# Kernel optimization log

Hardware: AMD Instinct MI355X
Metric: run time of the kernel (lower is better)

The kernel has to match this reference:

```python
import jax, jax.numpy as jnp
import numpy as np

N, C_IN, T, V = 128, 64, 64, 25
K = 3           # num_subsets
C_OUT = 192
MID = 64        # int((1/K) * C_OUT)
EPS = 1e-5


def conv1x1(x, W, b):
    # x: (n,c,t,v), W: (o,c), b: (o,)  -> (n,o,t,v)
    return jnp.einsum('nctv,oc->notv', x, W) + b[None, :, None, None]


def bn_eval(x, p):
    # p: (4,C) rows = gamma, beta, running_mean, running_var
    g, b, m, v = p[0], p[1], p[2], p[3]
    scale = (g * jax.lax.rsqrt(v + EPS))[None, :, None, None]
    return x * scale + (b - m * g * jax.lax.rsqrt(v + EPS))[None, :, None, None]


def _bn_params(key, c):
    kg, kb, km, kv = jax.random.split(key, 4)
    return jnp.stack([
        1.0 + 0.1 * jax.random.normal(kg, (c,), jnp.float32),
        0.1 * jax.random.normal(kb, (c,), jnp.float32),
        0.1 * jax.random.normal(km, (c,), jnp.float32),
        0.5 + jax.random.uniform(kv, (c,), jnp.float32),
    ])


def setup_inputs() -> dict:
    key = jax.random.key(0)
    ks = jax.random.split(key, 20)
    rn = lambda k, shape, s=1.0: s * jax.random.normal(k, shape, jnp.float32)
    return {
        'x': rn(ks[0], (N, C_IN, T, V)),
        'A': rn(ks[1], (K, V, V), 0.1),
        'alpha': rn(ks[2], (K,), 0.1),
        'beta': rn(ks[3], (K,), 0.1),
        'W_pre': rn(ks[4], (MID * K, C_IN), 0.05), 'b_pre': rn(ks[5], (MID * K,), 0.05),
        'bn_pre': _bn_params(ks[6], MID * K),
        'W1': rn(ks[7], (MID * K, C_IN), 0.05), 'b1': rn(ks[8], (MID * K,), 0.05),
        'W2': rn(ks[9], (MID * K, C_IN), 0.05), 'b2': rn(ks[10], (MID * K,), 0.05),
        'W_post': rn(ks[11], (C_OUT, MID * K), 0.05), 'b_post': rn(ks[12], (C_OUT,), 0.05),
        'bn_post': _bn_params(ks[13], C_OUT),
        'W_down': rn(ks[14], (C_OUT, C_IN), 0.05), 'b_down': rn(ks[15], (C_OUT,), 0.05),
        'bn_down': _bn_params(ks[16], C_OUT),
    }


def reference(x, A, alpha, beta, W_pre, b_pre, bn_pre, W1, b1, W2, b2,
              W_post, b_post, bn_post, W_down, b_down, bn_down):
    n = x.shape[0]
    # residual branch (in_channels != out_channels -> conv + BN)
    res = bn_eval(conv1x1(x, W_down, b_down), bn_down)
    # pre: conv1x1 -> BN -> ReLU, reshaped to (n,k,mid,t,v)
    pre_x = jax.nn.relu(bn_eval(conv1x1(x, W_pre, b_pre), bn_pre)).reshape(n, K, MID, T, V)
    # ctr/ada both active and neither 'NA' -> temporal mean
    tmp = x.mean(axis=2, keepdims=True)                      # (n,c,1,v)
    x1 = conv1x1(tmp, W1, b1).reshape(n, K, MID, 1, V)       # (n,k,mid,1,v)
    x2 = conv1x1(tmp, W2, b2).reshape(n, K, MID, 1, V)
    # ctr branch: tanh(pairwise diff) * alpha[0], added to static A
    diff = jnp.tanh(x1[..., :, None] - x2[..., None, :]) * alpha[0]   # (n,k,mid,1,v,v)
    Adyn = diff + A[None, :, None, None]                              # broadcast (1,k,1,1,v,v)
    # ada branch: softmax(x1^T x2) over axis -2, scaled by beta[0]
    ada = jnp.einsum('nkctv,nkctw->nktvw', x1, x2)[:, :, None]        # (n,k,1,1,v,v)
    ada = jax.nn.softmax(ada, axis=-2) * beta[0]
    Adyn = Adyn + ada                                                 # (n,k,mid,1,v,v)
    # A.shape[3] == 1 path: squeeze t-dim, channel-wise adjacency
    Adyn = Adyn[:, :, :, 0]                                           # (n,k,mid,v,v)
    y = jnp.einsum('nkctv,nkcvw->nkctw', pre_x, Adyn).reshape(n, K * MID, T, V)
    y = conv1x1(y, W_post, b_post)
    return jax.nn.relu(bn_eval(y, bn_post) + res)
```

## Files before the change

kernel.cpp:

```cpp
#include <hip/hip_runtime.h>
#include <hip/hip_bf16.h>

typedef __hip_bfloat16 bf16;
typedef __attribute__((ext_vector_type(8))) short s16x8;
typedef __attribute__((ext_vector_type(4))) float f32x4;

constexpr int cN = 128, cC = 64, cT = 64, cV = 25, cK = 3, cMID = 64, cKM = 192, cTV = 1600;
constexpr float cEPS = 1e-5f;

__device__ float g_tmp[cN * cC * cV];
__device__ ushort g_adF[(size_t)cN * cKM * 1024];
__device__ ushort g_WpreF[2 * 12 * 512];
__device__ ushort g_WcatF[8 * 12 * 512];
__device__ float g_bpre [cKM];
__device__ float g_cterm[cKM];

__device__ __forceinline__ ushort f2bu(float v){ return __builtin_bit_cast(ushort, __float2bfloat16(v)); }

__device__ __forceinline__ int zidx(int oct, int col){
  return (oct*128 + (col ^ ((oct & 3) << 1))) * 8;
}

__global__ __launch_bounds__(256) void gm_tmp(const float* __restrict__ x,
    const float* __restrict__ Wpre, const float* __restrict__ bpre,
    const float* __restrict__ bnpre,
    const float* __restrict__ Wpost, const float* __restrict__ bpost,
    const float* __restrict__ bnpost,
    const float* __restrict__ Wdown, const float* __restrict__ bdown,
    const float* __restrict__ bndown){
  __shared__ float xs[4 * cTV];
  int n = blockIdx.x >> 4, cg = blockIdx.x & 15;
  int tid = threadIdx.x;
  const float* xp = x + ((size_t)n*cC + cg*4)*cTV;
  for (int i = tid; i < 4*cTV; i += 256) xs[i] = xp[i];
  __syncthreads();
  if (tid < 100){
    int c = tid / 25, v = tid - c*25;
    float s = 0.f;
    #pragma unroll
    for (int t = 0; t < cT; ++t) s += xs[c*cTV + t*cV + v];
    g_tmp[(n*cC + cg*4 + c)*cV + v] = s * (1.f/cT);
  }
  if (blockIdx.x >= 8) return;
  __syncthreads();
  float* sPre  = xs;
  float* sPost = xs + 32;
  float* sDown = xs + 64;
  int ob = blockIdx.x * 24;
  if (tid < 24){
    int o = ob + tid;
    float sp = bnpre[o] * rsqrtf(bnpre[3*cKM+o] + cEPS);
    sPre[tid] = sp;
    g_bpre[o] = bpre[o]*sp + bnpre[cKM+o] - bnpre[2*cKM+o]*sp;
    float sP = bnpost[o] * rsqrtf(bnpost[3*cKM+o] + cEPS);
    float sD = bndown[o] * rsqrtf(bndown[3*cKM+o] + cEPS);
    sPost[tid] = sP; sDown[tid] = sD;
    g_cterm[o] = bpost[o]*sP + bnpost[cKM+o] - bnpost[2*cKM+o]*sP
               + bdown[o]*sD + bndown[cKM+o] - bndown[2*cKM+o]*sD;
  }
  __syncthreads();
  for (int i = tid; i < 24*cC; i += 256){
    int ol = i >> 6, k = i & 63;
    int o = ob + ol;
    int step = k >> 5, g = (k >> 3) & 3, j = k & 7;
    int dst = ((step*12 + (o>>4)) << 9) + (((g<<4) | (o&15)) << 3) + j;
    g_WpreF[dst] = f2bu(Wpre[o*cC + k] * sPre[ol]);
  }
  for (int i = tid; i < 24*256; i += 256){
    int ol = i >> 8, k = i & 255;
    int o = ob + ol;
    float w = (k < cKM) ? Wpost[o*cKM + k] * sPost[ol]
                        : Wdown[o*cC + (k - cKM)] * sDown[ol];
    int step = k >> 5, g = (k >> 3) & 3, j = k & 7;
    int dst = ((step*12 + (o>>4)) << 9) + (((g<<4) | (o&15)) << 3) + j;
    g_WcatF[dst] = f2bu(w);
  }
}

__global__ __launch_bounds__(512) void gm_prep(
    const float* __restrict__ W1, const float* __restrict__ b1,
    const float* __restrict__ W2, const float* __restrict__ b2,
    const float* __restrict__ A,  const float* __restrict__ alpha,
    const float* __restrict__ beta){
  __shared__ float tl [cC*cV + 32];
  __shared__ float w1l[cMID*65];
  __shared__ float w2l[cMID*65];
  __shared__ float x1l[cMID*cV];
  __shared__ float x2l[cMID*cV];
  __shared__ float Al [cV*cV];
  __shared__ float adal[cV*cV];
  int bid = blockIdx.x; int n = bid / 3, kg = bid % 3;
  int tid = threadIdx.x;
  for (int i = tid; i < cC*cV; i += 512) tl[i] = g_tmp[n*cC*cV + i];
  if (tid < 32) tl[cC*cV + tid] = 0.f;
  for (int i = tid; i < cV*cV; i += 512) Al[i] = A[kg*625 + i];
  for (int i = tid; i < cMID*cC; i += 512){
    int ch = i >> 6, c = i & 63;
    w1l[ch*65 + c] = W1[(kg*cMID + ch)*cC + c];
    w2l[ch*65 + c] = W2[(kg*cMID + ch)*cC + c];
  }
  __syncthreads();
  {
    int ch = tid >> 3, iv = tid & 7;
    int o = kg*cMID + ch;
    float bb1 = b1[o], bb2 = b2[o];
    float s1[4] = {bb1, bb1, bb1, bb1};
    float s2[4] = {bb2, bb2, bb2, bb2};
    #pragma unroll 8
    for (int c = 0; c < cC; ++c){
      float w1c = w1l[ch*65 + c], w2c = w2l[ch*65 + c];
      #pragma unroll
      for (int k = 0; k < 4; ++k){
        float t = tl[c*cV + iv + 8*k];
        s1[k] += w1c * t;
        s2[k] += w2c * t;
      }
    }
    #pragma unroll
    for (int k = 0; k < 4; ++k){
      int v = iv + 8*k;
      if (v < cV){ x1l[ch*cV + v] = s1[k]; x2l[ch*cV + v] = s2[k]; }
    }
  }
  __syncthreads();
  for (int idx = tid; idx < cV*cV; idx += 512){
    int v = idx / cV, w = idx % cV;
    float s = 0.f;
    #pragma unroll 8
    for (int c = 0; c < cMID; ++c) s += x1l[c*cV + v] * x2l[c*cV + w];
    adal[idx] = s;
  }
  __syncthreads();
  float b0 = beta[0];
  if (tid < cV){
    int w = tid;
    float m = -1e30f;
    for (int v = 0; v < cV; ++v) m = fmaxf(m, adal[v*cV + w]);
    float s = 0.f;
    for (int v = 0; v < cV; ++v) s += __expf(adal[v*cV + w] - m);
    float inv = b0 / s;
    for (int v = 0; v < cV; ++v) adal[v*cV + w] = __expf(adal[v*cV + w] - m) * inv;
  }
  __syncthreads();
  for (int i = tid; i < cV*cV; i += 512) Al[i] += adal[i];
  __syncthreads();
  float a0 = alpha[0];
  int rem = tid * 2;
  int nf = rem >> 9, r2 = rem & 511;
  int li = r2 >> 3, j0 = r2 & 7;
  int v0 = 8*(li >> 4) + j0, w = 16*nf + (li & 15);
  bool wok = (w < cV);
  bool v0ok = wok && (v0 < cV), v1ok = wok && (v0 + 1 < cV);
  float AW0 = v0ok ? Al[v0*cV + w] : 0.f;
  float AW1 = v1ok ? Al[(v0+1)*cV + w] : 0.f;
  uint* dst = (uint*)(g_adF + ((size_t)n*cKM + kg*cMID)*1024 + rem);
  #pragma unroll 4
  for (int ch = 0; ch < cMID; ++ch){
    float f0 = 0.f, f1 = 0.f;
    if (wok){
      float xw = x2l[ch*cV + w];
      if (v0ok){
        float e2 = __expf(2.f*(x1l[ch*cV + v0] - xw));
        f0 = __fdividef(e2 - 1.f, e2 + 1.f)*a0 + AW0;
      }
      if (v1ok){
        float e2 = __expf(2.f*(x1l[ch*cV + v0 + 1] - xw));
        f1 = __fdividef(e2 - 1.f, e2 + 1.f)*a0 + AW1;
      }
    }
    dst[(size_t)ch * 512] = (uint)f2bu(f0) | ((uint)f2bu(f1) << 16);
  }
}

__global__ __launch_bounds__(512, 4) void gm_fused(const float* __restrict__ x,
                                                   float* __restrict__ outf){
  __shared__ ushort Zl[32 * 128 * 8];
  __shared__ ushort Pt[64 * 128];
  int c8 = (int)blockIdx.x & 7, i8 = (int)blockIdx.x >> 3;
  int n = c8 + 8*(i8 >> 4), ttile = i8 & 15;
  int t0 = ttile * 4;
  int tid = threadIdx.x;
  int wv = tid >> 6, lane = tid & 63, g = lane >> 4, l15 = lane & 15;
  int mfh = wv >> 1;
  int nfh = wv & 1;

  #pragma unroll
  for (int s0 = 0; s0 < 1024; s0 += 512){
    int s = s0 + tid;
    int oct = 24 + (s >> 7), col = s & 127;
    int t = col >> 5, v = col & 31;
    ushort u[8];
    if (v < cV){
      const float* xp = x + ((size_t)n*cC + (oct-24)*8)*cTV + (t0 + t)*cV + v;
      #pragma unroll
      for (int j = 0; j < 8; ++j) u[j] = f2bu(xp[(size_t)j*cTV]);
    } else {
      #pragma unroll
      for (int j = 0; j < 8; ++j) u[j] = 0;
    }
    *(uint4*)&Zl[zidx(oct, col)] = *(const uint4*)u;
  }

  #pragma unroll 1
  for (int kg = 0; kg < 3; ++kg){
    __syncthreads();
    s16x8 bva0[8], bva1[8];
    #pragma unroll
    for (int cc = 0; cc < 8; ++cc){
      const ushort* bp = g_adF + ((size_t)n*cKM + kg*64 + wv*8 + cc)*1024;
      bva0[cc] = *(const s16x8*)(bp + lane*8);
      bva1[cc] = *(const s16x8*)(bp + 512 + lane*8);
    }
    f32x4 a1[4];
    #pragma unroll
    for (int nn = 0; nn < 4; ++nn) a1[nn] = (f32x4){0.f,0.f,0.f,0.f};
    #pragma unroll
    for (int ks = 0; ks < 2; ++ks){
      s16x8 av = *(const s16x8*)(g_WpreF + ((ks*12 + kg*4 + mfh) << 9) + lane*8);
      #pragma unroll
      for (int nn = 0; nn < 4; ++nn){
        int col = 16*(nfh*4 + nn) + l15;
        s16x8 bv = *(const s16x8*)&Zl[zidx(24 + ks*4 + g, col)];
        a1[nn] = __builtin_amdgcn_mfma_f32_16x16x32_bf16(av, bv, a1[nn], 0, 0, 0);
      }
    }
    #pragma unroll
    for (int nn = 0; nn < 4; ++nn){
      int col = 16*(nfh*4 + nn) + l15;
      int t = col >> 5, v = col & 31;
      #pragma unroll
      for (int q = 0; q < 4; ++q){
        int o = 16*mfh + 4*g + q;
        float val = (v < cV) ? fmaxf(a1[nn][q] + g_bpre[kg*64 + o], 0.f) : 0.f;
        int slot = ((v>>3) ^ (o>>2)) & 3;
        Pt[o*128 + slot*32 + t*8 + (v & 7)] = f2bu(val);
      }
    }
    __syncthreads();
    int octY = kg*8 + wv;
    #pragma unroll
    for (int cc = 0; cc < 8; cc += 2){
      int chlE = wv*8 + cc, chlO = chlE + 1;
      s16x8 avE, avO;
      if (l15 < 4){
        int slotE = (g ^ (chlE>>2)) & 3;
        avE = *(const s16x8*)&Pt[chlE*128 + slotE*32 + l15*8];
        avO = *(const s16x8*)&Pt[chlO*128 + slotE*32 + l15*8];
      } else { avE = (s16x8){0,0,0,0,0,0,0,0}; avO = avE; }
      f32x4 d0e = __builtin_amdgcn_mfma_f32_16x16x32_bf16(avE, bva0[cc],   (f32x4){0.f,0.f,0.f,0.f}, 0, 0, 0);
      f32x4 d1e = __builtin_amdgcn_mfma_f32_16x16x32_bf16(avE, bva1[cc],   (f32x4){0.f,0.f,0.f,0.f}, 0, 0, 0);
      f32x4 d0o = __builtin_amdgcn_mfma_f32_16x16x32_bf16(avO, bva0[cc+1], (f32x4){0.f,0.f,0.f,0.f}, 0, 0, 0);
      f32x4 d1o = __builtin_amdgcn_mfma_f32_16x16x32_bf16(avO, bva1[cc+1], (f32x4){0.f,0.f,0.f,0.f}, 0, 0, 0);
      if (g == 0){
        #pragma unroll
        for (int q = 0; q < 4; ++q){
          uint p0 = (uint)f2bu(d0e[q]) | ((uint)f2bu(d0o[q]) << 16);
          uint p1 = (uint)f2bu(d1e[q]) | ((uint)f2bu(d1o[q]) << 16);
          *(uint*)&Zl[zidx(octY, q*32 + l15)      + cc] = p0;
          *(uint*)&Zl[zidx(octY, q*32 + 16 + l15) + cc] = p1;
        }
      }
    }
  }
  __syncthreads();
  f32x4 a3[3][4];
  #pragma unroll
  for (int mm = 0; mm < 3; ++mm)
    #pragma unroll
    for (int nn = 0; nn < 4; ++nn) a3[mm][nn] = (f32x4){0.f,0.f,0.f,0.f};
  s16x8 avc[3], avn[3];
  #pragma unroll
  for (int mm = 0; mm < 3; ++mm)
    avc[mm] = *(const s16x8*)(g_WcatF + ((0*12 + mfh*3 + mm) << 9) + lane*8);
  #pragma unroll 1
  for (int ks = 0; ks < 8; ++ks){
    if (ks < 7){
      #pragma unroll
      for (int mm = 0; mm < 3; ++mm)
        avn[mm] = *(const s16x8*)(g_WcatF + (((ks+1)*12 + mfh*3 + mm) << 9) + lane*8);
    }
    s16x8 bv[4];
    #pragma unroll
    for (int nn = 0; nn < 4; ++nn){
      int col = 16*(nfh*4 + nn) + l15;
      bv[nn] = *(const s16x8*)&Zl[zidx(ks*4 + g, col)];
    }
    #pragma unroll
    for (int mm = 0; mm < 3; ++mm)
      #pragma unroll
      for (int nn = 0; nn < 4; ++nn)
        a3[mm][nn] = __builtin_amdgcn_mfma_f32_16x16x32_bf16(avc[mm], bv[nn], a3[mm][nn], 0, 0, 0);
    #pragma unroll
    for (int mm = 0; mm < 3; ++mm) avc[mm] = avn[mm];
  }
  #pragma unroll
  for (int mm = 0; mm < 3; ++mm){
    #pragma unroll
    for (int q = 0; q < 4; ++q){
      int o = 48*mfh + 16*mm + 4*g + q;
      float ct = g_cterm[o];
      #pragma unroll
      for (int nn = 0; nn < 4; ++nn){
        int col = 16*(nfh*4 + nn) + l15;
        int t = col >> 5, v = col & 31;
        if (v < cV)
          outf[((size_t)n*cKM + o)*cTV + (t0 + t)*cV + v] = fmaxf(a3[mm][nn][q] + ct, 0.f);
      }
    }
  }
}

extern "C" void kernel_launch(void* const* d_in, const int* in_sizes, int n_in,
                              void* d_out, int out_size, void* d_ws, size_t ws_size,
                              hipStream_t stream){
  (void)in_sizes; (void)n_in; (void)out_size; (void)d_ws; (void)ws_size;
  const float* x      = (const float*)d_in[0];
  const float* A      = (const float*)d_in[1];
  const float* alpha  = (const float*)d_in[2];
  const float* beta   = (const float*)d_in[3];
  const float* W_pre  = (const float*)d_in[4];
  const float* b_pre  = (const float*)d_in[5];
  const float* bn_pre = (const float*)d_in[6];
  const float* W1     = (const float*)d_in[7];
  const float* b1     = (const float*)d_in[8];
  const float* W2     = (const float*)d_in[9];
  const float* b2     = (const float*)d_in[10];
  const float* W_post = (const float*)d_in[11];
  const float* b_post = (const float*)d_in[12];
  const float* bn_post= (const float*)d_in[13];
  const float* W_down = (const float*)d_in[14];
  const float* b_down = (const float*)d_in[15];
  const float* bn_down= (const float*)d_in[16];
  float* out = (float*)d_out;

  gm_tmp  <<<cN * 16,  256, 0, stream>>>(x, W_pre, b_pre, bn_pre,
                                         W_post, b_post, bn_post,
                                         W_down, b_down, bn_down);
  gm_prep <<<cN * 3,   512, 0, stream>>>(W1, b1, W2, b2, A, alpha, beta);
  gm_fused<<<cN * 16,  512, 0, stream>>>(x, out);
}
```

Measured before the change: 161.1 us.

## Interleave post-conv accumulation per subset to halve LDS and raise occupancy

The final post-conv GEMM now accumulates incrementally after each subset's graph aggregation, so only one subset's Y octets plus the x octets have to stay in LDS. This halves the Zl buffer and lets launch bounds request 6 blocks per CU instead of 4. The second half of the adjacency B fragments is now loaded inside the aggregation loop rather than prefetched, which lowers register pressure. In exchange, the a3 accumulators stay live for the whole kernel, each subset needs an extra barrier, and the weight-prefetch pipelining of the old post loop is gone, so register spills or longer latency stalls are possible.

```diff
diff --git a/kernel.cpp b/kernel.cpp
--- a/kernel.cpp
+++ b/kernel.cpp
@@ -172,9 +172,9 @@
   }
 }
 
-__global__ __launch_bounds__(512, 4) void gm_fused(const float* __restrict__ x,
+__global__ __launch_bounds__(512, 6) void gm_fused(const float* __restrict__ x,
                                                    float* __restrict__ outf){
-  __shared__ ushort Zl[32 * 128 * 8];
+  __shared__ ushort Zl[16 * 128 * 8];
   __shared__ ushort Pt[64 * 128];
   int c8 = (int)blockIdx.x & 7, i8 = (int)blockIdx.x >> 3;
   int n = c8 + 8*(i8 >> 4), ttile = i8 & 15;
@@ -187,11 +187,11 @@
   #pragma unroll
   for (int s0 = 0; s0 < 1024; s0 += 512){
     int s = s0 + tid;
-    int oct = 24 + (s >> 7), col = s & 127;
+    int oct = 8 + (s >> 7), col = s & 127;
     int t = col >> 5, v = col & 31;
     ushort u[8];
     if (v < cV){
-      const float* xp = x + ((size_t)n*cC + (oct-24)*8)*cTV + (t0 + t)*cV + v;
+      const float* xp = x + ((size_t)n*cC + (oct-8)*8)*cTV + (t0 + t)*cV + v;
       #pragma unroll
       for (int j = 0; j < 8; ++j) u[j] = f2bu(xp[(size_t)j*cTV]);
     } else {
@@ -200,17 +200,21 @@
     }
     *(uint4*)&Zl[zidx(oct, col)] = *(const uint4*)u;
   }
+
+  f32x4 a3[3][4];
+  #pragma unroll
+  for (int mm = 0; mm < 3; ++mm)
+    #pragma unroll
+    for (int nn = 0; nn < 4; ++nn) a3[mm][nn] = (f32x4){0.f,0.f,0.f,0.f};
 
   #pragma unroll 1
   for (int kg = 0; kg < 3; ++kg){
     __syncthreads();
-    s16x8 bva0[8], bva1[8];
-    #pragma unroll
-    for (int cc = 0; cc < 8; ++cc){
-      const ushort* bp = g_adF + ((size_t)n*cKM + kg*64 + wv*8 + cc)*1024;
-      bva0[cc] = *(const s16x8*)(bp + lane*8);
-      bva1[cc] = *(const s16x8*)(bp + 512 + lane*8);
-    }
+    const ushort* bpBase = g_adF + ((size_t)n*cKM + kg*64 + wv*8)*1024;
+    s16x8 bva0[8];
+    #pragma unroll
+    for (int cc = 0; cc < 8; ++cc)
+      bva0[cc] = *(const s16x8*)(bpBase + cc*1024 + lane*8);
     f32x4 a1[4];
     #pragma unroll
     for (int nn = 0; nn < 4; ++nn) a1[nn] = (f32x4){0.f,0.f,0.f,0.f};
@@ -220,7 +224,7 @@
       #pragma unroll
       for (int nn = 0; nn < 4; ++nn){
         int col = 16*(nfh*4 + nn) + l15;
-        s16x8 bv = *(const s16x8*)&Zl[zidx(24 + ks*4 + g, col)];
+        s16x8 bv = *(const s16x8*)&Zl[zidx(8 + ks*4 + g, col)];
         a1[nn] = __builtin_amdgcn_mfma_f32_16x16x32_bf16(av, bv, a1[nn], 0, 0, 0);
       }
     }
@@ -237,7 +241,6 @@
       }
     }
     __syncthreads();
-    int octY = kg*8 + wv;
     #pragma unroll
     for (int cc = 0; cc < 8; cc += 2){
       int chlE = wv*8 + cc, chlO = chlE + 1;
@@ -247,51 +250,59 @@
         avE = *(const s16x8*)&Pt[chlE*128 + slotE*32 + l15*8];
         avO = *(const s16x8*)&Pt[chlO*128 + slotE*32 + l15*8];
       } else { avE = (s16x8){0,0,0,0,0,0,0,0}; avO = avE; }
+      s16x8 b1e = *(const s16x8*)(bpBase + cc*1024     + 512 + lane*8);
+      s16x8 b1o = *(const s16x8*)(bpBase + (cc+1)*1024 + 512 + lane*8);
       f32x4 d0e = __builtin_amdgcn_mfma_f32_16x16x32_bf16(avE, bva0[cc],   (f32x4){0.f,0.f,0.f,0.f}, 0, 0, 0);
-      f32x4 d1e = __builtin_amdgcn_mfma_f32_16x16x32_bf16(avE, bva1[cc],   (f32x4){0.f,0.f,0.f,0.f}, 0, 0, 0);
+      f32x4 d1e = __builtin_amdgcn_mfma_f32_16x16x32_bf16(avE, b1e,        (f32x4){0.f,0.f,0.f,0.f}, 0, 0, 0);
       f32x4 d0o = __builtin_amdgcn_mfma_f32_16x16x32_bf16(avO, bva0[cc+1], (f32x4){0.f,0.f,0.f,0.f}, 0, 0, 0);
-      f32x4 d1o = __builtin_amdgcn_mfma_f32_16x16x32_bf16(avO, bva1[cc+1], (f32x4){0.f,0.f,0.f,0.f}, 0, 0, 0);
+      f32x4 d1o = __builtin_amdgcn_mfma_f32_16x16x32_bf16(avO, b1o,        (f32x4){0.f,0.f,0.f,0.f}, 0, 0, 0);
       if (g == 0){
         #pragma unroll
         for (int q = 0; q < 4; ++q){
           uint p0 = (uint)f2bu(d0e[q]) | ((uint)f2bu(d0o[q]) << 16);
           uint p1 = (uint)f2bu(d1e[q]) | ((uint)f2bu(d1o[q]) << 16);
-          *(uint*)&Zl[zidx(octY, q*32 + l15)      + cc] = p0;
-          *(uint*)&Zl[zidx(octY, q*32 + 16 + l15) + cc] = p1;
+          *(uint*)&Zl[zidx(wv, q*32 + l15)      + cc] = p0;
+          *(uint*)&Zl[zidx(wv, q*32 + 16 + l15) + cc] = p1;
         }
       }
     }
-  }
-  __syncthreads();
-  f32x4 a3[3][4];
+    __syncthreads();
+    #pragma unroll
+    for (int ks2 = 0; ks2 < 2; ++ks2){
+      int ks3 = kg*2 + ks2;
+      s16x8 avc[3], bv[4];
+      #pragma unroll
+      for (int mm = 0; mm < 3; ++mm)
+        avc[mm] = *(const s16x8*)(g_WcatF + ((ks3*12 + mfh*3 + mm) << 9) + lane*8);
+      #pragma unroll
+      for (int nn = 0; nn < 4; ++nn){
+        int col = 16*(nfh*4 + nn) + l15;
+        bv[nn] = *(const s16x8*)&Zl[zidx(ks2*4 + g, col)];
+      }
+      #pragma unroll
+      for (int mm = 0; mm < 3; ++mm)
+        #pragma unroll
+        for (int nn = 0; nn < 4; ++nn)
+          a3[mm][nn] = __builtin_amdgcn_mfma_f32_16x16x32_bf16(avc[mm], bv[nn], a3[mm][nn], 0, 0, 0);
+    }
+  }
   #pragma unroll
-  for (int mm = 0; mm < 3; ++mm)
-    #pragma unroll
-    for (int nn = 0; nn < 4; ++nn) a3[mm][nn] = (f32x4){0.f,0.f,0.f,0.f};
-  s16x8 avc[3], avn[3];
-  #pragma unroll
-  for (int mm = 0; mm < 3; ++mm)
-    avc[mm] = *(const s16x8*)(g_WcatF + ((0*12 + mfh*3 + mm) << 9) + lane*8);
-  #pragma unroll 1
-  for (int ks = 0; ks < 8; ++ks){
-    if (ks < 7){
-      #pragma unroll
-      for (int mm = 0; mm < 3; ++mm)
-        avn[mm] = *(const s16x8*)(g_WcatF + (((ks+1)*12 + mfh*3 + mm) << 9) + lane*8);
-    }
-    s16x8 bv[4];
+  for (int ks2 = 0; ks2 < 2; ++ks2){
+    int ks3 = 6 + ks2;
+    s16x8 avc[3], bv[4];
+    #pragma unroll
+    for (int mm = 0; mm < 3; ++mm)
+      avc[mm] = *(const s16x8*)(g_WcatF + ((ks3*12 + mfh*3 + mm) << 9) + lane*8);
     #pragma unroll
     for (int nn = 0; nn < 4; ++nn){
       int col = 16*(nfh*4 + nn) + l15;
-      bv[nn] = *(const s16x8*)&Zl[zidx(ks*4 + g, col)];
+      bv[nn] = *(const s16x8*)&Zl[zidx(8 + ks2*4 + g, col)];
     }
     #pragma unroll
     for (int mm = 0; mm < 3; ++mm)
       #pragma unroll
       for (int nn = 0; nn < 4; ++nn)
         a3[mm][nn] = __builtin_amdgcn_mfma_f32_16x16x32_bf16(avc[mm], bv[nn], a3[mm][nn], 0, 0, 0);
-    #pragma unroll
-    for (int mm = 0; mm < 3; ++mm) avc[mm] = avn[mm];
   }
   #pragma unroll
   for (int mm = 0; mm < 3; ++mm){
```

After: 498.7 us. 3.1x slower.
